# Performance work log

Hardware: AMD Instinct MI355X
Metric: run time of the kernel (lower is better)

Reference implementation:

```python
import jax, jax.numpy as jnp
import numpy as np
from jax import lax

N = 20000        # nodes
E = 320000       # directed edges (avg degree 16)
F_IN = 512       # input feature dim
HID = 64         # hidden_layer
K_NEI = 8        # sampled neighbors per node
L = K_NEI + 1    # local subgraph size (self + neighbors)
N_TPL = 10       # N_templates
NT = 8           # N_templates_nodes
N_CLS = 6
ALPHA = 0.5      # FGW trade-off
EPS = 0.1        # entropic regularization
N_OUTER = 3      # outer CG iterations
N_SINK = 5       # sinkhorn iterations per outer step


def setup_inputs() -> dict:
    rng = np.random.default_rng(0)
    src = rng.integers(0, N, E).astype(np.int64)
    dst = rng.integers(0, N, E).astype(np.int64)
    edge_index = np.stack([src, dst])

    # fixed-size neighbor table (pad with self, mask)
    nbr = np.full((N, K_NEI), -1, np.int64)
    cnt = np.zeros(N, np.int64)
    for s, d in zip(src, dst):
        c = cnt[s]
        if c < K_NEI:
            nbr[s, c] = d
            cnt[s] = c + 1
    pad = nbr < 0
    self_col = np.arange(N, dtype=np.int64)
    nbr = np.where(pad, self_col[:, None], nbr)
    nbr_mask = np.concatenate([np.ones((N, 1)), (~pad).astype(np.float64)], 1).astype(np.float32)

    # local adjacency among {self, neighbors}: [N, L, L]
    idx_full = np.concatenate([self_col[:, None], nbr], 1)  # [N, L]
    edge_keys = np.unique(src * N + dst)
    keys = idx_full[:, :, None] * N + idx_full[:, None, :]
    C_local = np.isin(keys, edge_keys).astype(np.float32)

    ks = jax.random.split(jax.random.key(0), 10)
    x = jax.random.normal(ks[0], (N, F_IN), jnp.float32)
    W1 = jax.random.normal(ks[1], (F_IN, HID), jnp.float32) / np.float32(np.sqrt(F_IN))
    b1 = jnp.zeros((HID,), jnp.float32)
    W2 = jax.random.normal(ks[2], (HID, HID), jnp.float32) / np.float32(np.sqrt(HID))
    b2 = jnp.zeros((HID,), jnp.float32)
    t = jax.random.uniform(ks[3], (N_TPL, NT, NT), jnp.float32)
    templates = 0.5 * (t + jnp.swapaxes(t, 1, 2))  # symmetric template adjacency
    templates_features = jax.random.normal(ks[4], (N_TPL, NT, HID), jnp.float32)
    Wlin = jax.random.normal(ks[5], (HID + N_TPL, N_CLS), jnp.float32) / np.float32(np.sqrt(HID + N_TPL))
    blin = jnp.zeros((N_CLS,), jnp.float32)
    return {"x": x, "edge_index": jnp.asarray(edge_index), "nbr_idx": jnp.asarray(nbr),
            "nbr_mask": jnp.asarray(nbr_mask), "C_local": jnp.asarray(C_local),
            "W1": W1, "b1": b1, "W2": W2, "b2": b2,
            "templates": templates, "templates_features": templates_features,
            "Wlin": Wlin, "blin": blin}


def gcn(x, W, b, src, dst, n):
    xw = x @ W
    sl = jnp.arange(n)
    s = jnp.concatenate([src, sl])
    d = jnp.concatenate([dst, sl])
    deg = jax.ops.segment_sum(jnp.ones_like(s, jnp.float32), d, num_segments=n)
    dinv = lax.rsqrt(deg)
    coef = dinv[s] * dinv[d]
    return jax.ops.segment_sum(xw[s] * coef[:, None], d, num_segments=n) + b


def fgw_dist(M, C1, h1, C2, h2):
    # entropic fused GW (square loss) with fixed iterations; padded rows have h1 = 0
    f1 = C1 * C1
    f2 = C2 * C2
    constC = (f1 @ h1)[:, None] + (f2 @ h2)[None, :]
    T0 = h1[:, None] * h2[None, :]

    def outer(T, _):
        tens = constC - 2.0 * (C1 @ T @ C2)
        G = (1.0 - ALPHA) * M + ALPHA * tens
        Kmat = jnp.exp(-G / EPS)

        def sink(carry, _):
            u, v = carry
            u = h1 / (Kmat @ v + 1e-16)
            v = h2 / (Kmat.T @ u + 1e-16)
            return (u, v), None

        (u, v), _ = lax.scan(sink, (jnp.ones_like(h1), jnp.ones_like(h2)), None, length=N_SINK)
        return u[:, None] * Kmat * v[None, :], None

    T, _ = lax.scan(outer, T0, None, length=N_OUTER)
    tens = constC - 2.0 * (C1 @ T @ C2)
    return jnp.sum(T * ((1.0 - ALPHA) * M + ALPHA * tens))


def distance_to_template(x, nbr_idx, nbr_mask, C_local, templates_features, templates):
    n = x.shape[0]
    idx_full = jnp.concatenate([jnp.arange(n)[:, None], nbr_idx], axis=1)  # [N, L]
    xl = x[idx_full]  # [N, L, HID]
    # squared euclidean cost to each template: [N, T, L, NT]
    inner = jnp.einsum('nld,tmd->ntlm', xl, templates_features)
    M = (jnp.sum(xl * xl, -1)[:, None, :, None]
         + jnp.sum(templates_features * templates_features, -1)[None, :, None, :]
         - 2.0 * inner)
    h1 = nbr_mask / jnp.sum(nbr_mask, -1, keepdims=True)  # [N, L]
    h2 = jnp.full((NT,), 1.0 / NT, jnp.float32)

    per_tpl = jax.vmap(fgw_dist, in_axes=(0, None, None, 0, None))
    per_node = jax.vmap(per_tpl, in_axes=(0, 0, 0, None, None))
    return per_node(M, C_local, h1, templates, h2)  # [N, N_TPL]


def reference(x, edge_index, nbr_idx, nbr_mask, C_local, W1, b1, W2, b2,
              templates, templates_features, Wlin, blin):
    src, dst = edge_index[0], edge_index[1]
    n = x.shape[0]
    h = jax.nn.relu(gcn(x, W1, b1, src, dst, n))
    h = gcn(h, W2, b2, src, dst, n)
    y = distance_to_template(h, nbr_idx, nbr_mask, C_local, templates_features, templates)
    out = jnp.concatenate([h, y], axis=1) @ Wlin + blin
    return jax.nn.relu(out)
```

## Files before the change

### kernel.cpp

```cpp
#include <hip/hip_runtime.h>


#define NN   20000
#define EE   320000
#define FIN  512
#define HID  64
#define KNEI 8
#define LSZ  9
#define NTPL 10
#define NTN  8
#define NCLS 6
#define CAP  48

typedef unsigned short bf16_t;
typedef unsigned short us8 __attribute__((ext_vector_type(8)));

__device__ __forceinline__ float b2f(bf16_t u) {
  union { unsigned int i; float f; } v; v.i = ((unsigned int)u) << 16; return v.f;
}
__device__ __forceinline__ bf16_t f2b(float f) {
  union { float f; unsigned int i; } v; v.f = f;
  unsigned int x = v.i;
  return (bf16_t)((x + 0x7fffu + ((x >> 16) & 1u)) >> 16);
}
__device__ __forceinline__ float ldf(const void* p, long i, int fp32) {
  return fp32 ? ((const float*)p)[i] : b2f(((const bf16_t*)p)[i]);
}
__device__ __forceinline__ int ldi(const void* p, long i, int i64) {
  return i64 ? (int)((const long long*)p)[i] : ((const int*)p)[i];
}
__device__ __forceinline__ float frcp(float x) { return __builtin_amdgcn_rcpf(x); }

__global__ __launch_bounds__(128) void probe_kernel(const void* __restrict__ x,
                                                    const void* __restrict__ ei,
                                                    const void* __restrict__ tfeat,
                                                    int* __restrict__ flags,
                                                    float* __restrict__ tn2min) {
  __shared__ int sfl[2];
  __shared__ float tn2s[80];
  int tid = threadIdx.x;
  if (tid == 0) {
    int sane = 0;
    for (int k = 0; k < 64; k += 2) {
      bf16_t u = ((const bf16_t*)x)[k];
      int e = (u >> 7) & 0xff;
      if (e >= 112 && e <= 142) sane++;
    }
    int f0 = (sane < 24) ? 1 : 0;
    int zc = 0;
    for (int k = 1; k < 64; k += 2)
      if (((const int*)ei)[k] == 0) zc++;
    int f1 = (zc >= 16) ? 1 : 0;
    flags[0] = f0; flags[1] = f1;
    sfl[0] = f0; sfl[1] = f1;
  }
  __syncthreads();
  if (tid < 80) {
    int fF = sfl[0];
    float s = 0.f;
    for (int k = 0; k < HID; ++k) {
      float v = ldf(tfeat, (long)tid * HID + k, fF);
      s += v * v;
    }
    tn2s[tid] = s;
  }
  __syncthreads();
  if (tid == 0) {
    float gmin = 1e30f;
    for (int t = 0; t < NTPL; ++t) {
      float m = tn2s[t * 8];
      for (int r = 1; r < 8; ++r) m = fminf(m, tn2s[t * 8 + r]);
      tn2min[t] = m;
      gmin = fminf(gmin, m);
    }
    tn2min[NTPL] = gmin;
  }
}

__global__ __launch_bounds__(256) void scatter_kernel(const void* __restrict__ ei,
                                                      int* __restrict__ pos,
                                                      int* __restrict__ slot,
                                                      const int* __restrict__ flags) {
  int i = blockIdx.x * 256 + threadIdx.x;
  if (i >= EE) return;
  int i64 = flags[1];
  int s = ldi(ei, i, i64);
  int d = ldi(ei, (long)EE + i, i64);
  int p = atomicAdd(&pos[d], 1);
  if (p < CAP) slot[d * CAP + p] = s;
}

__global__ __launch_bounds__(256) void gemm1_kernel(const void* __restrict__ x,
                                                    const void* __restrict__ W1,
                                                    float* __restrict__ xw1,
                                                    const int* __restrict__ flags) {
  int wave = blockIdx.x * 4 + (threadIdx.x >> 6);
  int lane = threadIdx.x & 63;
  int row0 = wave * 4;
  if (row0 >= NN) return;
  float a0 = 0.f, a1 = 0.f, a2 = 0.f, a3 = 0.f;
  if (!flags[0]) {
    const bf16_t* xb = (const bf16_t*)x + (long)row0 * FIN;
    const bf16_t* wp = (const bf16_t*)W1;
#pragma unroll 2
    for (int k8 = 0; k8 < FIN / 8; ++k8) {
      us8 r0 = *(const us8*)(xb + k8 * 8);
      us8 r1 = *(const us8*)(xb + FIN + k8 * 8);
      us8 r2 = *(const us8*)(xb + 2 * FIN + k8 * 8);
      us8 r3 = *(const us8*)(xb + 3 * FIN + k8 * 8);
#pragma unroll
      for (int q = 0; q < 8; ++q) {
        float w = b2f(wp[(k8 * 8 + q) * HID + lane]);
        a0 += b2f(r0[q]) * w;
        a1 += b2f(r1[q]) * w;
        a2 += b2f(r2[q]) * w;
        a3 += b2f(r3[q]) * w;
      }
    }
  } else {
    const float* x0 = (const float*)x + (long)row0 * FIN;
    const float* wp = (const float*)W1;
#pragma unroll 8
    for (int k = 0; k < FIN; ++k) {
      float w = wp[k * HID + lane];
      a0 += x0[k] * w;
      a1 += x0[FIN + k] * w;
      a2 += x0[2 * FIN + k] * w;
      a3 += x0[3 * FIN + k] * w;
    }
  }
  xw1[(long)(row0 + 0) * HID + lane] = a0;
  xw1[(long)(row0 + 1) * HID + lane] = a1;
  xw1[(long)(row0 + 2) * HID + lane] = a2;
  xw1[(long)(row0 + 3) * HID + lane] = a3;
}

__global__ __launch_bounds__(256) void gatherA_kernel(const float* __restrict__ xw,
                                                      const int* __restrict__ cnt,
                                                      const int* __restrict__ slot,
                                                      float* __restrict__ xw2,
                                                      const void* __restrict__ b1v,
                                                      const void* __restrict__ W2,
                                                      const int* __restrict__ flags) {
  int n = blockIdx.x * 4 + (threadIdx.x >> 6);
  if (n >= NN) return;
  int fF = flags[0];
  int c = threadIdx.x & 63;
  float dn = rsqrtf((float)cnt[n] + 1.0f);
  float acc = xw[(long)n * HID + c] * dn;
  int m = cnt[n]; if (m > CAP) m = CAP;
  const int* sl = slot + (long)n * CAP;
  float accB = 0.f;
  for (int e0 = 0; e0 < m; e0 += 8) {
    int4 sa = *(const int4*)(sl + e0);
    int4 sb = *(const int4*)(sl + e0 + 4);
    if (e0 + 0 < m) acc  += xw[(long)sa.x * HID + c] * rsqrtf((float)cnt[sa.x] + 1.0f);
    if (e0 + 1 < m) accB += xw[(long)sa.y * HID + c] * rsqrtf((float)cnt[sa.y] + 1.0f);
    if (e0 + 2 < m) acc  += xw[(long)sa.z * HID + c] * rsqrtf((float)cnt[sa.z] + 1.0f);
    if (e0 + 3 < m) accB += xw[(long)sa.w * HID + c] * rsqrtf((float)cnt[sa.w] + 1.0f);
    if (e0 + 4 < m) acc  += xw[(long)sb.x * HID + c] * rsqrtf((float)cnt[sb.x] + 1.0f);
    if (e0 + 5 < m) accB += xw[(long)sb.y * HID + c] * rsqrtf((float)cnt[sb.y] + 1.0f);
    if (e0 + 6 < m) acc  += xw[(long)sb.z * HID + c] * rsqrtf((float)cnt[sb.z] + 1.0f);
    if (e0 + 7 < m) accB += xw[(long)sb.w * HID + c] * rsqrtf((float)cnt[sb.w] + 1.0f);
  }
  float h1 = (acc + accB) * dn + ldf(b1v, c, fF);
  h1 = h1 > 0.f ? h1 : 0.f;

  float o = 0.f;
#pragma unroll 8
  for (int k = 0; k < HID; ++k)
    o += __shfl(h1, k) * ldf(W2, k * HID + c, fF);
  xw2[(long)n * HID + c] = o;
}

__global__ __launch_bounds__(256) void gatherB_kernel(const float* __restrict__ xw,
                                                      const int* __restrict__ cnt,
                                                      const int* __restrict__ slot,
                                                      float* __restrict__ h,
                                                      float* __restrict__ n2,
                                                      const void* __restrict__ b2v,
                                                      const int* __restrict__ flags) {
  int n = blockIdx.x * 4 + (threadIdx.x >> 6);
  if (n >= NN) return;
  int c = threadIdx.x & 63;
  float dn = rsqrtf((float)cnt[n] + 1.0f);
  float acc = xw[(long)n * HID + c] * dn;
  int m = cnt[n]; if (m > CAP) m = CAP;
  const int* sl = slot + (long)n * CAP;
  float accB = 0.f;
  for (int e0 = 0; e0 < m; e0 += 8) {
    int4 sa = *(const int4*)(sl + e0);
    int4 sb = *(const int4*)(sl + e0 + 4);
    if (e0 + 0 < m) acc  += xw[(long)sa.x * HID + c] * rsqrtf((float)cnt[sa.x] + 1.0f);
    if (e0 + 1 < m) accB += xw[(long)sa.y * HID + c] * rsqrtf((float)cnt[sa.y] + 1.0f);
    if (e0 + 2 < m) acc  += xw[(long)sa.z * HID + c] * rsqrtf((float)cnt[sa.z] + 1.0f);
    if (e0 + 3 < m) accB += xw[(long)sa.w * HID + c] * rsqrtf((float)cnt[sa.w] + 1.0f);
    if (e0 + 4 < m) acc  += xw[(long)sb.x * HID + c] * rsqrtf((float)cnt[sb.x] + 1.0f);
    if (e0 + 5 < m) accB += xw[(long)sb.y * HID + c] * rsqrtf((float)cnt[sb.y] + 1.0f);
    if (e0 + 6 < m) acc  += xw[(long)sb.z * HID + c] * rsqrtf((float)cnt[sb.z] + 1.0f);
    if (e0 + 7 < m) accB += xw[(long)sb.w * HID + c] * rsqrtf((float)cnt[sb.w] + 1.0f);
  }
  acc = (acc + accB) * dn;
  h[(long)n * HID + c] = acc;
  float v = acc + ldf(b2v, c, flags[0]);
  float s = v * v;
  s += __shfl_xor(s, 1); s += __shfl_xor(s, 2); s += __shfl_xor(s, 4);
  s += __shfl_xor(s, 8); s += __shfl_xor(s, 16); s += __shfl_xor(s, 32);
  if (c == 0) n2[n] = s;
}

#define NODES_PB 4
#define TPN 80
#define XLP 65

__global__ __launch_bounds__(320, 2) void fgw_kernel(
    const float* __restrict__ h2,
    const void* __restrict__ b2v,
    const void* __restrict__ nbr_idx,
    const void* __restrict__ nbr_mask,
    const void* __restrict__ C_local,
    const void* __restrict__ tmpl,
    const void* __restrict__ tfeat,
    const void* __restrict__ Wlin,
    const void* __restrict__ blin,
    void* __restrict__ out,
    const int* __restrict__ flags,
    const float* __restrict__ tn2min,
    const float* __restrict__ n2)
{
  const int tid = threadIdx.x;
  const int fF = flags[0];
  const int fI = flags[1];
  const int nb = tid / TPN;
  const int local = tid - nb * TPN;
  const int t = local >> 3;
  const int j = local & 7;
  const int n = blockIdx.x * NODES_PB + nb;
  const int lane = tid & 63;
  const int ob = lane & 56;

  __shared__ float xlS[NODES_PB][LSZ][XLP];
  __shared__ float C1S[NODES_PB][81];
  __shared__ float hwS[NODES_PB][LSZ];
  __shared__ float f1S[NODES_PB][LSZ];
  __shared__ float xnS[NODES_PB][LSZ];
  __shared__ float distS[NODES_PB][NTPL];
  __shared__ float xmaxS[NODES_PB];
  __shared__ int   needS[NODES_PB];
  __shared__ int   sidxS[NODES_PB][LSZ];
  __shared__ float WlinS[(HID + NTPL) * NCLS + NCLS];

  for (int i = tid; i < (HID + NTPL) * NCLS; i += 320)
    WlinS[i] = ldf(Wlin, i, fF);
  if (tid < NCLS) WlinS[(HID + NTPL) * NCLS + tid] = ldf(blin, tid, fF);

  if (local < LSZ) {
    int idx = (local == 0) ? n : ldi(nbr_idx, (long)n * KNEI + local - 1, fI);
    sidxS[nb][local] = idx;
    xnS[nb][local] = n2[idx];
  }
  if (local < HID)
    xlS[nb][0][local] = h2[(long)n * HID + local] + ldf(b2v, local, fF);
  __syncthreads();

  if (local == 0) {
    float xm = xnS[nb][0];
#pragma unroll
    for (int l = 1; l < LSZ; ++l) xm = fmaxf(xm, xnS[nb][l]);
    xmaxS[nb] = xm;
    needS[nb] = ((sqrtf(tn2min[NTPL]) - sqrtf(xm)) >= 5.0990195f) ? 0 : 1;
  }
  __syncthreads();

  const int need = needS[nb];
  if (need) {
    for (int i = local; i < 8 * HID; i += TPN) {
      int l = 1 + (i >> 6), k = i & 63;
      xlS[nb][l][k] = h2[(long)sidxS[nb][l] * HID + k] + ldf(b2v, k, fF);
    }
    for (int i = local; i < 81; i += TPN)
      C1S[nb][i] = ldf(C_local, (long)n * 81 + i, fF);
  }
  __syncthreads();

  if (need && local < LSZ) {
    int l = local;
    float msum = 0.f, f1 = 0.f;
#pragma unroll
    for (int jj = 0; jj < LSZ; ++jj) {
      float mj = ldf(nbr_mask, (long)n * LSZ + jj, fF);
      msum += mj;
      float c = C1S[nb][l * LSZ + jj];
      f1 += c * c * mj;
    }
    float inv = frcp(msum);
    hwS[nb][l] = ldf(nbr_mask, (long)n * LSZ + l, fF) * inv;
    f1S[nb][l] = f1 * inv;
  }
  __syncthreads();

  bool slow = need && ((sqrtf(tn2min[t]) - sqrtf(xmaxS[nb])) < 5.0990195f);
  if (slow) {
    float C2c[NTN];
    float f2h2;
    {
      float s = 0.f;
#pragma unroll
      for (int m = 0; m < NTN; ++m) {
        C2c[m] = ldf(tmpl, t * 64 + m * 8 + j, fF);
        float r = ldf(tmpl, t * 64 + j * 8 + m, fF);
        s += r * r;
      }
      f2h2 = s * 0.125f;
    }
    float hwr[LSZ], f1r[LSZ];
#pragma unroll
    for (int l = 0; l < LSZ; ++l) { hwr[l] = hwS[nb][l]; f1r[l] = f1S[nb][l]; }

    float Mc[LSZ];
    {
      float accI[LSZ];
#pragma unroll
      for (int l = 0; l < LSZ; ++l) accI[l] = 0.f;
      float tn2 = 0.f;
      const long tb = (long)local * HID;
      for (int kb = 0; kb < 8; ++kb) {
        float r[8];
#pragma unroll
        for (int q = 0; q < 8; ++q) r[q] = ldf(tfeat, tb + kb * 8 + q, fF);
#pragma unroll
        for (int q = 0; q < 8; ++q) tn2 += r[q] * r[q];
#pragma unroll
        for (int l = 0; l < LSZ; ++l) {
          float s = 0.f;
#pragma unroll
          for (int q = 0; q < 8; ++q) s += xlS[nb][l][kb * 8 + q] * r[q];
          accI[l] += s;
        }
      }
#pragma unroll
      for (int l = 0; l < LSZ; ++l)
        Mc[l] = xnS[nb][l] + tn2 - 2.f * accI[l];
    }

    float Tc[LSZ], Kc[LSZ], u[LSZ];
#pragma unroll
    for (int l = 0; l < LSZ; ++l) Tc[l] = hwr[l] * 0.125f;

    float v = 1.0f;
    for (int outer = 0; outer < 3; ++outer) {
      float Ac[LSZ];
#pragma unroll
      for (int l = 0; l < LSZ; ++l) {
        float s = 0.f;
#pragma unroll
        for (int l2 = 0; l2 < LSZ; ++l2) s += C1S[nb][l * LSZ + l2] * Tc[l2];
        Ac[l] = s;
      }
#pragma unroll
      for (int l = 0; l < LSZ; ++l) {
        float s = 0.f;
#pragma unroll
        for (int m = 0; m < NTN; ++m) s += __shfl(Ac[l], ob + m) * C2c[m];
        float tens = f1r[l] + f2h2 - 2.f * s;
        Kc[l] = __expf(-5.0f * (Mc[l] + tens));
      }
      v = 1.0f;
      for (int it = 0; it < 5; ++it) {
#pragma unroll
        for (int l = 0; l < LSZ; ++l) {
          float p = Kc[l] * v;
          p += __shfl_xor(p, 1); p += __shfl_xor(p, 2); p += __shfl_xor(p, 4);
          u[l] = hwr[l] * frcp(p + 1e-16f);
        }
        float s = 0.f;
#pragma unroll
        for (int l = 0; l < LSZ; ++l) s += Kc[l] * u[l];
        v = 0.125f * frcp(s + 1e-16f);
      }
#pragma unroll
      for (int l = 0; l < LSZ; ++l) Tc[l] = u[l] * Kc[l] * v;
    }
    {
      float Ac[LSZ];
#pragma unroll
      for (int l = 0; l < LSZ; ++l) {
        float s = 0.f;
#pragma unroll
        for (int l2 = 0; l2 < LSZ; ++l2) s += C1S[nb][l * LSZ + l2] * Tc[l2];
        Ac[l] = s;
      }
      float cl = 0.f;
#pragma unroll
      for (int l = 0; l < LSZ; ++l) {
        float s = 0.f;
#pragma unroll
        for (int m = 0; m < NTN; ++m) s += __shfl(Ac[l], ob + m) * C2c[m];
        float tens = f1r[l] + f2h2 - 2.f * s;
        cl += Tc[l] * 0.5f * (Mc[l] + tens);
      }
      cl += __shfl_xor(cl, 1); cl += __shfl_xor(cl, 2); cl += __shfl_xor(cl, 4);
      if (j == 0) distS[nb][t] = cl;
    }
  } else if (j == 0) {
    distS[nb][t] = 0.f;
  }
  __syncthreads();

  if (local < NCLS) {
    int c = local;
    float acc = WlinS[(HID + NTPL) * NCLS + c];
#pragma unroll
    for (int k = 0; k < HID; ++k)
      acc += xlS[nb][0][k] * WlinS[k * NCLS + c];
#pragma unroll
    for (int tt = 0; tt < NTPL; ++tt)
      acc += distS[nb][tt] * WlinS[(HID + tt) * NCLS + c];
    float r = acc > 0.f ? acc : 0.f;
    if (fF) ((float*)out)[(long)n * NCLS + c] = r;
    else    ((bf16_t*)out)[(long)n * NCLS + c] = f2b(r);
  }
}

extern "C" void kernel_launch(void* const* d_in, const int* in_sizes, int n_in,
                              void* d_out, int out_size, void* d_ws, size_t ws_size,
                              hipStream_t stream) {
  (void)in_sizes; (void)n_in; (void)out_size; (void)ws_size;
  const void* x     = d_in[0];
  const void* ei    = d_in[1];
  const void* nbr   = d_in[2];
  const void* nmask = d_in[3];
  const void* Cl    = d_in[4];
  const void* W1    = d_in[5];
  const void* b1    = d_in[6];
  const void* W2    = d_in[7];
  const void* b2    = d_in[8];
  const void* tmpl  = d_in[9];
  const void* tfeat = d_in[10];
  const void* Wlin  = d_in[11];
  const void* blin  = d_in[12];

  int*   flags  = (int*)d_ws;
  float* tn2min = (float*)d_ws + 4;
  float* n2     = (float*)d_ws + 16;
  int*   pos    = (int*)(n2 + NN);
  int*   slot   = pos + NN;
  float* bufA   = (float*)(slot + (long)CAP * NN);
  float* bufB   = bufA + (long)NN * HID;

  probe_kernel<<<1, 128, 0, stream>>>(x, ei, tfeat, flags, tn2min);

  hipMemsetAsync(pos, 0, NN * sizeof(int), stream);
  scatter_kernel<<<(EE + 255) / 256, 256, 0, stream>>>(ei, pos, slot, flags);

  gemm1_kernel<<<NN / 16, 256, 0, stream>>>(x, W1, bufA, flags);
  gatherA_kernel<<<NN / 4, 256, 0, stream>>>(bufA, pos, slot, bufB, b1, W2, flags);
  gatherB_kernel<<<NN / 4, 256, 0, stream>>>(bufB, pos, slot, bufA, n2, b2, flags);

  fgw_kernel<<<NN / NODES_PB, 320, 0, stream>>>(bufA, b2, nbr, nmask, Cl, tmpl,
                                                tfeat, Wlin, blin, d_out, flags,
                                                tn2min, n2);
}
```

Before: 317.1 us.

## Use MFMA bf16 matrix cores for first GCN GEMM with LDS-staged weights

Rewrites the x@W1 projection for the bf16 path to use 16x16x32 bf16 MFMA instructions. W1 is transposed into XOR-swizzled shared memory and each wave keeps its 16-column weight slice in registers. The grid becomes persistent: 256 blocks of 512 threads stride over 16-row tiles. The goal is to replace the scalar FMA loop, which is compute-bound, with matrix-core throughput. In exchange the kernel needs 64KB of LDS and a weight transpose in every block, and the fp32 fallback now uses a grid-stride loop.

```diff
diff --git a/kernel.cpp b/kernel.cpp
--- a/kernel.cpp
+++ b/kernel.cpp
@@ -14,6 +14,8 @@
 
 typedef unsigned short bf16_t;
 typedef unsigned short us8 __attribute__((ext_vector_type(8)));
+typedef __bf16 bf16x8 __attribute__((ext_vector_type(8)));
+typedef float f32x4 __attribute__((ext_vector_type(4)));
 
 __device__ __forceinline__ float b2f(bf16_t u) {
   union { unsigned int i; float f; } v; v.i = ((unsigned int)u) << 16; return v.f;
@@ -90,49 +92,75 @@
   if (p < CAP) slot[d * CAP + p] = s;
 }
 
-__global__ __launch_bounds__(256) void gemm1_kernel(const void* __restrict__ x,
+__global__ __launch_bounds__(512) void gemm1_kernel(const void* __restrict__ x,
                                                     const void* __restrict__ W1,
                                                     float* __restrict__ xw1,
                                                     const int* __restrict__ flags) {
-  int wave = blockIdx.x * 4 + (threadIdx.x >> 6);
-  int lane = threadIdx.x & 63;
-  int row0 = wave * 4;
-  if (row0 >= NN) return;
-  float a0 = 0.f, a1 = 0.f, a2 = 0.f, a3 = 0.f;
-  if (!flags[0]) {
-    const bf16_t* xb = (const bf16_t*)x + (long)row0 * FIN;
-    const bf16_t* wp = (const bf16_t*)W1;
-#pragma unroll 2
-    for (int k8 = 0; k8 < FIN / 8; ++k8) {
-      us8 r0 = *(const us8*)(xb + k8 * 8);
-      us8 r1 = *(const us8*)(xb + FIN + k8 * 8);
-      us8 r2 = *(const us8*)(xb + 2 * FIN + k8 * 8);
-      us8 r3 = *(const us8*)(xb + 3 * FIN + k8 * 8);
-#pragma unroll
-      for (int q = 0; q < 8; ++q) {
-        float w = b2f(wp[(k8 * 8 + q) * HID + lane]);
-        a0 += b2f(r0[q]) * w;
-        a1 += b2f(r1[q]) * w;
-        a2 += b2f(r2[q]) * w;
-        a3 += b2f(r3[q]) * w;
-      }
+  const int tid = threadIdx.x;
+  const int wid = tid >> 6;
+  const int lane = tid & 63;
+  const int fF = flags[0];
+
+  if (!fF) {
+    __shared__ bf16_t wtS[HID * FIN];
+    for (int i = tid; i < (FIN * HID) / 8; i += 512) {
+      us8 v = ((const us8*)W1)[i];
+      int k = i >> 3;
+      int c0 = (i & 7) * 8;
+#pragma unroll
+      for (int q = 0; q < 8; ++q)
+        wtS[(c0 + q) * FIN + (k ^ (q << 3))] = v[q];
+    }
+    __syncthreads();
+
+    const int ct = wid & 3;
+    const int ws = blockIdx.x * 2 + (wid >> 2);
+    const int lr = lane & 15;
+    const int lg = lane >> 4;
+
+    bf16x8 af[16];
+#pragma unroll
+    for (int s = 0; s < 16; ++s) {
+      int idx8 = (ct * 16 + lr) * (FIN / 8) + ((4 * s + lg) ^ (lane & 7));
+      union { us8 u; bf16x8 b; } t;
+      t.u = *(const us8*)&wtS[idx8 * 8];
+      af[s] = t.b;
+    }
+
+    for (int rb = ws; rb < NN / 16; rb += 512) {
+      const int row = rb * 16 + lr;
+      const bf16x8* xp = (const bf16x8*)x + (long)row * (FIN / 8) + lg;
+      f32x4 acc0 = {0.f, 0.f, 0.f, 0.f};
+      f32x4 acc1 = {0.f, 0.f, 0.f, 0.f};
+#pragma unroll
+      for (int s = 0; s < 16; s += 2) {
+        bf16x8 b0 = xp[4 * s];
+        bf16x8 b1 = xp[4 * s + 4];
+        acc0 = __builtin_amdgcn_mfma_f32_16x16x32_bf16(af[s], b0, acc0, 0, 0, 0);
+        acc1 = __builtin_amdgcn_mfma_f32_16x16x32_bf16(af[s + 1], b1, acc1, 0, 0, 0);
+      }
+      f32x4 r = acc0 + acc1;
+      *(f32x4*)&xw1[(long)row * HID + ct * 16 + lg * 4] = r;
     }
   } else {
-    const float* x0 = (const float*)x + (long)row0 * FIN;
-    const float* wp = (const float*)W1;
+    for (int row0 = (blockIdx.x * 8 + wid) * 4; row0 < NN; row0 += 2048 * 4) {
+      float a0 = 0.f, a1 = 0.f, a2 = 0.f, a3 = 0.f;
+      const float* x0 = (const float*)x + (long)row0 * FIN;
+      const float* wp = (const float*)W1;
 #pragma unroll 8
-    for (int k = 0; k < FIN; ++k) {
-      float w = wp[k * HID + lane];
-      a0 += x0[k] * w;
-      a1 += x0[FIN + k] * w;
-      a2 += x0[2 * FIN + k] * w;
-      a3 += x0[3 * FIN + k] * w;
-    }
-  }
-  xw1[(long)(row0 + 0) * HID + lane] = a0;
-  xw1[(long)(row0 + 1) * HID + lane] = a1;
-  xw1[(long)(row0 + 2) * HID + lane] = a2;
-  xw1[(long)(row0 + 3) * HID + lane] = a3;
+      for (int k = 0; k < FIN; ++k) {
+        float w = wp[k * HID + lane];
+        a0 += x0[k] * w;
+        a1 += x0[FIN + k] * w;
+        a2 += x0[2 * FIN + k] * w;
+        a3 += x0[3 * FIN + k] * w;
+      }
+      xw1[(long)(row0 + 0) * HID + lane] = a0;
+      xw1[(long)(row0 + 1) * HID + lane] = a1;
+      xw1[(long)(row0 + 2) * HID + lane] = a2;
+      xw1[(long)(row0 + 3) * HID + lane] = a3;
+    }
+  }
 }
 
 __global__ __launch_bounds__(256) void gatherA_kernel(const float* __restrict__ xw,
@@ -453,7 +481,7 @@
   hipMemsetAsync(pos, 0, NN * sizeof(int), stream);
   scatter_kernel<<<(EE + 255) / 256, 256, 0, stream>>>(ei, pos, slot, flags);
 
-  gemm1_kernel<<<NN / 16, 256, 0, stream>>>(x, W1, bufA, flags);
+  gemm1_kernel<<<256, 512, 0, stream>>>(x, W1, bufA, flags);
   gatherA_kernel<<<NN / 4, 256, 0, stream>>>(bufA, pos, slot, bufB, b1, W2, flags);
   gatherB_kernel<<<NN / 4, 256, 0, stream>>>(bufB, pos, slot, bufA, n2, b2, flags);
 
```

After: 335.1 us. +5.7%, slower.

## Prescale GCN features by degree norm and fold pos reset into probe

Applied to the files above, without the earlier changes.

Each row of the GEMM outputs (xw1 in gemm1, xw2 in gatherA) is multiplied by its own rsqrt(degree+1) factor when written. The two gather kernels then just sum neighbour rows and apply the destination norm once, with no per-edge count load or rsqrt. The separate memset of the position counters becomes a grid-stride zeroing pass inside a widened probe kernel, which saves one launch. It also adds a device-to-device copy of x into the workspace before gemm1, apparently for locality, but this extra traffic could cost more than it saves.

```diff
diff --git a/kernel.cpp b/kernel.cpp
--- a/kernel.cpp
+++ b/kernel.cpp
@@ -31,14 +31,19 @@
 }
 __device__ __forceinline__ float frcp(float x) { return __builtin_amdgcn_rcpf(x); }
 
-__global__ __launch_bounds__(128) void probe_kernel(const void* __restrict__ x,
+__global__ __launch_bounds__(256) void probe_kernel(const void* __restrict__ x,
                                                     const void* __restrict__ ei,
                                                     const void* __restrict__ tfeat,
                                                     int* __restrict__ flags,
-                                                    float* __restrict__ tn2min) {
+                                                    float* __restrict__ tn2min,
+                                                    int* __restrict__ pos) {
+  int tid = threadIdx.x;
+  int zi = blockIdx.x * 256 + tid;
+  if (zi < NN) pos[zi] = 0;
+  if (blockIdx.x != 0) return;
+
   __shared__ int sfl[2];
   __shared__ float tn2s[80];
-  int tid = threadIdx.x;
   if (tid == 0) {
     int sane = 0;
     for (int k = 0; k < 64; k += 2) {
@@ -92,6 +97,7 @@
 
 __global__ __launch_bounds__(256) void gemm1_kernel(const void* __restrict__ x,
                                                     const void* __restrict__ W1,
+                                                    const int* __restrict__ cnt,
                                                     float* __restrict__ xw1,
                                                     const int* __restrict__ flags) {
   int wave = blockIdx.x * 4 + (threadIdx.x >> 6);
@@ -129,16 +135,20 @@
       a3 += x0[3 * FIN + k] * w;
     }
   }
-  xw1[(long)(row0 + 0) * HID + lane] = a0;
-  xw1[(long)(row0 + 1) * HID + lane] = a1;
-  xw1[(long)(row0 + 2) * HID + lane] = a2;
-  xw1[(long)(row0 + 3) * HID + lane] = a3;
-}
-
-__global__ __launch_bounds__(256) void gatherA_kernel(const float* __restrict__ xw,
+  float d0 = rsqrtf((float)cnt[row0 + 0] + 1.0f);
+  float d1 = rsqrtf((float)cnt[row0 + 1] + 1.0f);
+  float d2 = rsqrtf((float)cnt[row0 + 2] + 1.0f);
+  float d3 = rsqrtf((float)cnt[row0 + 3] + 1.0f);
+  xw1[(long)(row0 + 0) * HID + lane] = a0 * d0;
+  xw1[(long)(row0 + 1) * HID + lane] = a1 * d1;
+  xw1[(long)(row0 + 2) * HID + lane] = a2 * d2;
+  xw1[(long)(row0 + 3) * HID + lane] = a3 * d3;
+}
+
+__global__ __launch_bounds__(256) void gatherA_kernel(const float* __restrict__ sxw,
                                                       const int* __restrict__ cnt,
                                                       const int* __restrict__ slot,
-                                                      float* __restrict__ xw2,
+                                                      float* __restrict__ sxw2,
                                                       const void* __restrict__ b1v,
                                                       const void* __restrict__ W2,
                                                       const int* __restrict__ flags) {
@@ -146,23 +156,23 @@
   if (n >= NN) return;
   int fF = flags[0];
   int c = threadIdx.x & 63;
-  float dn = rsqrtf((float)cnt[n] + 1.0f);
-  float acc = xw[(long)n * HID + c] * dn;
+  float acc = sxw[(long)n * HID + c];
   int m = cnt[n]; if (m > CAP) m = CAP;
   const int* sl = slot + (long)n * CAP;
   float accB = 0.f;
   for (int e0 = 0; e0 < m; e0 += 8) {
     int4 sa = *(const int4*)(sl + e0);
     int4 sb = *(const int4*)(sl + e0 + 4);
-    if (e0 + 0 < m) acc  += xw[(long)sa.x * HID + c] * rsqrtf((float)cnt[sa.x] + 1.0f);
-    if (e0 + 1 < m) accB += xw[(long)sa.y * HID + c] * rsqrtf((float)cnt[sa.y] + 1.0f);
-    if (e0 + 2 < m) acc  += xw[(long)sa.z * HID + c] * rsqrtf((float)cnt[sa.z] + 1.0f);
-    if (e0 + 3 < m) accB += xw[(long)sa.w * HID + c] * rsqrtf((float)cnt[sa.w] + 1.0f);
-    if (e0 + 4 < m) acc  += xw[(long)sb.x * HID + c] * rsqrtf((float)cnt[sb.x] + 1.0f);
-    if (e0 + 5 < m) accB += xw[(long)sb.y * HID + c] * rsqrtf((float)cnt[sb.y] + 1.0f);
-    if (e0 + 6 < m) acc  += xw[(long)sb.z * HID + c] * rsqrtf((float)cnt[sb.z] + 1.0f);
-    if (e0 + 7 < m) accB += xw[(long)sb.w * HID + c] * rsqrtf((float)cnt[sb.w] + 1.0f);
-  }
+    if (e0 + 0 < m) acc  += sxw[(long)sa.x * HID + c];
+    if (e0 + 1 < m) accB += sxw[(long)sa.y * HID + c];
+    if (e0 + 2 < m) acc  += sxw[(long)sa.z * HID + c];
+    if (e0 + 3 < m) accB += sxw[(long)sa.w * HID + c];
+    if (e0 + 4 < m) acc  += sxw[(long)sb.x * HID + c];
+    if (e0 + 5 < m) accB += sxw[(long)sb.y * HID + c];
+    if (e0 + 6 < m) acc  += sxw[(long)sb.z * HID + c];
+    if (e0 + 7 < m) accB += sxw[(long)sb.w * HID + c];
+  }
+  float dn = rsqrtf((float)cnt[n] + 1.0f);
   float h1 = (acc + accB) * dn + ldf(b1v, c, fF);
   h1 = h1 > 0.f ? h1 : 0.f;
 
@@ -170,10 +180,10 @@
 #pragma unroll 8
   for (int k = 0; k < HID; ++k)
     o += __shfl(h1, k) * ldf(W2, k * HID + c, fF);
-  xw2[(long)n * HID + c] = o;
-}
-
-__global__ __launch_bounds__(256) void gatherB_kernel(const float* __restrict__ xw,
+  sxw2[(long)n * HID + c] = o * dn;
+}
+
+__global__ __launch_bounds__(256) void gatherB_kernel(const float* __restrict__ sxw,
                                                       const int* __restrict__ cnt,
                                                       const int* __restrict__ slot,
                                                       float* __restrict__ h,
@@ -183,26 +193,26 @@
   int n = blockIdx.x * 4 + (threadIdx.x >> 6);
   if (n >= NN) return;
   int c = threadIdx.x & 63;
-  float dn = rsqrtf((float)cnt[n] + 1.0f);
-  float acc = xw[(long)n * HID + c] * dn;
+  float acc = sxw[(long)n * HID + c];
   int m = cnt[n]; if (m > CAP) m = CAP;
   const int* sl = slot + (long)n * CAP;
   float accB = 0.f;
   for (int e0 = 0; e0 < m; e0 += 8) {
     int4 sa = *(const int4*)(sl + e0);
     int4 sb = *(const int4*)(sl + e0 + 4);
-    if (e0 + 0 < m) acc  += xw[(long)sa.x * HID + c] * rsqrtf((float)cnt[sa.x] + 1.0f);
-    if (e0 + 1 < m) accB += xw[(long)sa.y * HID + c] * rsqrtf((float)cnt[sa.y] + 1.0f);
-    if (e0 + 2 < m) acc  += xw[(long)sa.z * HID + c] * rsqrtf((float)cnt[sa.z] + 1.0f);
-    if (e0 + 3 < m) accB += xw[(long)sa.w * HID + c] * rsqrtf((float)cnt[sa.w] + 1.0f);
-    if (e0 + 4 < m) acc  += xw[(long)sb.x * HID + c] * rsqrtf((float)cnt[sb.x] + 1.0f);
-    if (e0 + 5 < m) accB += xw[(long)sb.y * HID + c] * rsqrtf((float)cnt[sb.y] + 1.0f);
-    if (e0 + 6 < m) acc  += xw[(long)sb.z * HID + c] * rsqrtf((float)cnt[sb.z] + 1.0f);
-    if (e0 + 7 < m) accB += xw[(long)sb.w * HID + c] * rsqrtf((float)cnt[sb.w] + 1.0f);
-  }
-  acc = (acc + accB) * dn;
-  h[(long)n * HID + c] = acc;
-  float v = acc + ldf(b2v, c, flags[0]);
+    if (e0 + 0 < m) acc  += sxw[(long)sa.x * HID + c];
+    if (e0 + 1 < m) accB += sxw[(long)sa.y * HID + c];
+    if (e0 + 2 < m) acc  += sxw[(long)sa.z * HID + c];
+    if (e0 + 3 < m) accB += sxw[(long)sa.w * HID + c];
+    if (e0 + 4 < m) acc  += sxw[(long)sb.x * HID + c];
+    if (e0 + 5 < m) accB += sxw[(long)sb.y * HID + c];
+    if (e0 + 6 < m) acc  += sxw[(long)sb.z * HID + c];
+    if (e0 + 7 < m) accB += sxw[(long)sb.w * HID + c];
+  }
+  float dn = rsqrtf((float)cnt[n] + 1.0f);
+  float h2 = (acc + accB) * dn;
+  h[(long)n * HID + c] = h2;
+  float v = h2 + ldf(b2v, c, flags[0]);
   float s = v * v;
   s += __shfl_xor(s, 1); s += __shfl_xor(s, 2); s += __shfl_xor(s, 4);
   s += __shfl_xor(s, 8); s += __shfl_xor(s, 16); s += __shfl_xor(s, 32);
@@ -425,7 +435,7 @@
 extern "C" void kernel_launch(void* const* d_in, const int* in_sizes, int n_in,
                               void* d_out, int out_size, void* d_ws, size_t ws_size,
                               hipStream_t stream) {
-  (void)in_sizes; (void)n_in; (void)out_size; (void)ws_size;
+  (void)n_in; (void)out_size;
   const void* x     = d_in[0];
   const void* ei    = d_in[1];
   const void* nbr   = d_in[2];
@@ -440,20 +450,31 @@
   const void* Wlin  = d_in[11];
   const void* blin  = d_in[12];
 
-  int*   flags  = (int*)d_ws;
-  float* tn2min = (float*)d_ws + 4;
-  float* n2     = (float*)d_ws + 16;
-  int*   pos    = (int*)(n2 + NN);
-  int*   slot   = pos + NN;
-  float* bufA   = (float*)(slot + (long)CAP * NN);
-  float* bufB   = bufA + (long)NN * HID;
-
-  probe_kernel<<<1, 128, 0, stream>>>(x, ei, tfeat, flags, tn2min);
-
-  hipMemsetAsync(pos, 0, NN * sizeof(int), stream);
+  int*    flags  = (int*)d_ws;
+  float*  tn2min = (float*)d_ws + 4;
+  float*  n2     = (float*)d_ws + 16;
+  int*    pos    = (int*)(n2 + NN);
+  int*    slot   = pos + NN;
+  float*  bufA   = (float*)(slot + (long)CAP * NN);
+  float*  bufB   = bufA + (long)NN * HID;
+  void*   xc     = (void*)(bufB + (long)NN * HID);
+  const size_t BASE_BYTES = (size_t)(16 + 2 * NN + (long)CAP * NN
+                                     + 2 * (long)NN * HID) * 4;
+
+  const void* xsrc = x;
+  if (in_sizes) {
+    size_t s0 = (size_t)(unsigned)in_sizes[0];
+    if ((s0 == (size_t)NN * FIN * 2 || s0 == (size_t)NN * FIN * 4) &&
+        ws_size >= BASE_BYTES + s0) {
+      hipMemcpyAsync(xc, x, s0, hipMemcpyDeviceToDevice, stream);
+      xsrc = xc;
+    }
+  }
+
+  probe_kernel<<<79, 256, 0, stream>>>(x, ei, tfeat, flags, tn2min, pos);
   scatter_kernel<<<(EE + 255) / 256, 256, 0, stream>>>(ei, pos, slot, flags);
 
-  gemm1_kernel<<<NN / 16, 256, 0, stream>>>(x, W1, bufA, flags);
+  gemm1_kernel<<<NN / 16, 256, 0, stream>>>(xsrc, W1, pos, bufA, flags);
   gatherA_kernel<<<NN / 4, 256, 0, stream>>>(bufA, pos, slot, bufB, b1, W2, flags);
   gatherB_kernel<<<NN / 4, 256, 0, stream>>>(bufB, pos, slot, bufA, n2, b2, flags);
 
```

Result: no change. 314.0 us (-1.0%).
